# Kernel tuning notes

Measured on AMD Instinct MI355X. Metric: run time of the kernel, lower is better.

Reference implementation:

```python
import jax, jax.numpy as jnp
import numpy as np

C64 = jnp.complex64


def _rx(theta):
    # RX(t) = [[cos(t/2), -i sin(t/2)], [-i sin(t/2), cos(t/2)]]; theta scalar or [B]
    h = 0.5 * theta
    c = jnp.cos(h).astype(C64)
    s = (-1j * jnp.sin(h)).astype(C64)
    return jnp.stack([jnp.stack([c, s], -1), jnp.stack([s, c], -1)], -2)


def _ry(theta):
    h = 0.5 * theta
    c = jnp.cos(h).astype(C64)
    s = jnp.sin(h).astype(C64)
    return jnp.stack([jnp.stack([c, -s], -1), jnp.stack([s, c], -1)], -2)


def _rz(theta):
    h = 0.5 * theta
    em = jnp.exp(-1j * h).astype(C64)
    ep = jnp.exp(1j * h).astype(C64)
    z = jnp.zeros_like(em)
    return jnp.stack([jnp.stack([em, z], -1), jnp.stack([z, ep], -1)], -2)


def _apply_1q(state, U, q):
    # state: [B, 2^Q] complex; wire 0 is the most significant bit.
    B = state.shape[0]
    s = state.reshape(B, 2 ** q, 2, -1)
    if U.ndim == 3:  # batched gate [B,2,2]
        s = jnp.einsum('bij,bajc->baic', U, s)
    else:  # shared gate [2,2]
        s = jnp.einsum('ij,bajc->baic', U, s)
    return s.reshape(B, -1)


def _cnot_adj(state, q):
    # CNOT with control q, target q+1 (adjacent wires)
    B = state.shape[0]
    s = state.reshape(B, 2 ** q, 2, 2, -1)
    s = s.at[:, :, 1].set(s[:, :, 1, ::-1])
    return s.reshape(B, -1)


def _pqc(context, W, b, pqc_params):
    Q = W.shape[0]
    L = pqc_params.shape[0]
    angles = jnp.pi * jnp.tanh(context @ W.T + b)  # [B, Q]
    B = angles.shape[0]
    state = jnp.zeros((B, 2 ** Q), C64).at[:, 0].set(1.0)
    # data-encoding RX layer (batch-dependent angles)
    for q in range(Q):
        state = _apply_1q(state, _rx(angles[:, q]), q)
    # variational layers
    for l in range(L):
        for q in range(Q):
            state = _apply_1q(state, _rx(pqc_params[l, q, 0]), q)
            state = _apply_1q(state, _ry(pqc_params[l, q, 1]), q)
            state = _apply_1q(state, _rz(pqc_params[l, q, 2]), q)
        for q in range(Q - 1):
            state = _cnot_adj(state, q)
    # <Z_q> expectation for every wire
    probs = state.real ** 2 + state.imag ** 2  # [B, 2^Q]
    p = probs.reshape((B,) + (2,) * Q)
    z = [p.sum(tuple(i + 1 for i in range(Q) if i != q)) for q in range(Q)]  # each [B,2]
    z = jnp.stack(z, -1)  # [B, 2, Q] -> wait: stack of [B,2] on -1 -> [B,2,Q]
    return z[:, 0, :] - z[:, 1, :]  # [B, Q]


def setup_inputs() -> dict:
    key = jax.random.key(0)
    k0, k1, k2, k3 = jax.random.split(key, 4)
    B, D, Q, L = 512, 256, 16, 4
    context = jax.random.normal(k0, (B, D), jnp.float32)
    W = jax.random.normal(k1, (Q, D), jnp.float32) / np.float32(np.sqrt(D))
    b = 0.01 * jax.random.normal(k2, (Q,), jnp.float32)
    pqc_params = 0.01 * jax.random.normal(k3, (L, Q, 3), jnp.float32)
    return {"context": context, "W": W, "b": b, "pqc_params": pqc_params}


def reference(context, W, b, pqc_params):
    return _pqc(context, W, b, pqc_params)
```

## Files before the change

### kernel.cpp

```cpp
#include <hip/hip_runtime.h>
#include <math.h>

#define NQ   16
#define NTH  256
#define NB   512

typedef float2 c32;

__device__ __forceinline__ c32 cmul(c32 a, c32 b) {
    return make_float2(a.x*b.x - a.y*b.y, a.x*b.y + a.y*b.x);
}
__device__ __forceinline__ c32 cfma_(c32 a, c32 b, c32 acc) {
    acc.x = fmaf(a.x, b.x, fmaf(-a.y, b.y, acc.x));
    acc.y = fmaf(a.x, b.y, fmaf( a.y, b.x, acc.y));
    return acc;
}
__device__ __forceinline__ c32 cfmaConjA(c32 a, c32 b, c32 acc) {
    acc.x = fmaf(a.x, b.x, fmaf( a.y, b.y, acc.x));
    acc.y = fmaf(a.x, b.y, fmaf(-a.y, b.x, acc.y));
    return acc;
}
__device__ __forceinline__ c32 cmulConjA(c32 a, c32 b) {
    return cfmaConjA(a, b, make_float2(0.f, 0.f));
}
__device__ __forceinline__ c32 cadd(c32 a, c32 b){ return make_float2(a.x+b.x, a.y+b.y); }


__global__ __launch_bounds__(NTH, 2)
void pqc_mps_kernel(const float* __restrict__ ctx,
                    const float* __restrict__ Wm,
                    const float* __restrict__ bias,
                    const float* __restrict__ params,
                    float* __restrict__ out)
{
    __shared__ c32 Ac[14][272];
    __shared__ c32 A0c[16];
    __shared__ c32 A15v[32];
    __shared__ c32 Renv[15][144];
    __shared__ c32 Ssto[15][144];
    __shared__ c32 TR[272];
    __shared__ c32 TL[272];
    __shared__ c32 Lbuf[144];
    __shared__ c32 Ug[256];
    __shared__ c32 wv[64];
    __shared__ float angles[NQ];

    const int b = blockIdx.x;
    const int t = threadIdx.x;

    {
        const int q = t >> 4, g = t & 15;
        const float* crow = ctx + b * 256;
        const float* wrow = Wm + q * 256;
        float s = 0.f;
        #pragma unroll
        for (int j = 0; j < 16; ++j)
            s += crow[g + 16*j] * wrow[g + 16*j];
        #pragma unroll
        for (int m = 8; m; m >>= 1) s += __shfl_xor(s, m);
        if (g == 0) angles[q] = 3.14159265358979323846f * tanhf(s + bias[q]);
    }
    if (t < 64) {
        const float a  = params[t*3 + 0];
        const float bb = params[t*3 + 1];
        const float c  = params[t*3 + 2];
        const float ha = 0.5f*a, hb = 0.5f*bb, hc = 0.5f*c;
        const float ca = cosf(ha), sa = sinf(ha);
        const float cb = cosf(hb), sb = sinf(hb);
        const float cz = cosf(hc), sz = sinf(hc);
        const c32 m00 = make_float2( cb*ca,  sb*sa);
        const c32 m01 = make_float2(-sb*ca, -cb*sa);
        const c32 m10 = make_float2( sb*ca, -cb*sa);
        const c32 m11 = make_float2( cb*ca, -sb*sa);
        const c32 e0 = make_float2(cz, -sz);
        const c32 e1 = make_float2(cz,  sz);
        Ug[t*4 + 0] = cmul(e0, m00);
        Ug[t*4 + 1] = cmul(e0, m01);
        Ug[t*4 + 2] = cmul(e1, m10);
        Ug[t*4 + 3] = cmul(e1, m11);
    }
    __syncthreads();

    if (t < 64) {
        const int q = t >> 2, k = (t>>1)&1, i = t&1;
        const float h = 0.5f * angles[q];
        const float ch = cosf(h), sh = sinf(h);
        const int r0 = (i ^ k) << 1;
        const c32 u0 = Ug[(q<<2) + r0];
        const c32 u1 = Ug[(q<<2) + r0 + 1];
        wv[t] = make_float2(u0.x*ch + u1.y*sh, u0.y*ch - u1.x*sh);
    }
    __syncthreads();

    {
        const int r = t & 7, i = (t>>3)&1, a = t>>4;
        const int m0 = r&1, m1 = (r>>1)&1, m2 = r>>2;
        const int k0 = a&1, k1 = (a>>1)&1, k2 = (a>>2)&1, k3 = a>>3;
        #pragma unroll
        for (int q = 1; q <= 14; ++q) {
            const c32 u3 = Ug[((48+q)<<2) + ((i ^k3)<<1) + m2];
            const c32 u2 = Ug[((32+q)<<2) + ((m2^k2)<<1) + m1];
            const c32 u1 = Ug[((16+q)<<2) + ((m1^k1)<<1) + m0];
            const c32 ww = wv[(q<<2) + (k0<<1) + m0];
            Ac[q-1][a*17 + i*8 + r] = cmul(cmul(u3, u2), cmul(u1, ww));
        }
        if (t < 16) {
            const c32 u3 = Ug[(48<<2) + (i <<1) + m2];
            const c32 u2 = Ug[(32<<2) + (m2<<1) + m1];
            const c32 u1 = Ug[(16<<2) + (m1<<1) + m0];
            A0c[t] = cmul(cmul(u3, u2), cmul(u1, wv[m0]));
        }
        if (t >= 64 && t < 96) {
            const int idx = t - 64, aa = idx >> 1, ii = idx & 1;
            const int K0 = aa&1, K1 = (aa>>1)&1, K2 = (aa>>2)&1, K3 = aa>>3;
            c32 y1[2], y2[2];
            #pragma unroll
            for (int j1 = 0; j1 < 2; ++j1) {
                const int rr = (j1 ^ K1) << 1;
                y1[j1] = cfma_(Ug[((16+15)<<2)+rr], wv[60 + (K0<<1)],
                         cmul (Ug[((16+15)<<2)+rr+1], wv[60 + (K0<<1) + 1]));
            }
            #pragma unroll
            for (int j2 = 0; j2 < 2; ++j2) {
                const int rr = (j2 ^ K2) << 1;
                y2[j2] = cfma_(Ug[((32+15)<<2)+rr], y1[0],
                         cmul (Ug[((32+15)<<2)+rr+1], y1[1]));
            }
            const int rr = (ii ^ K3) << 1;
            A15v[(aa<<1)+ii] = cfma_(Ug[((48+15)<<2)+rr], y2[0],
                               cmul (Ug[((48+15)<<2)+rr+1], y2[1]));
        }
    }
    __syncthreads();

    if (t < 128) {
        const int m = t>>6, bl = (t>>3)&7, bp = t&7;
        c32 acc = cmulConjA(A15v[((m<<3)+bl)<<1],       A15v[((m<<3)+bp)<<1]);
        acc     = cfmaConjA(A15v[(((m<<3)+bl)<<1) + 1], A15v[(((m<<3)+bp)<<1) + 1], acc);
        Renv[14][m*72 + bl*9 + bp] = acc;
    } else {
        const int u = t-128, i = u>>6, bl = (u>>3)&7, bp = u&7;
        const c32 s = cmulConjA(A0c[(i<<3)+bl], A0c[(i<<3)+bp]);
        Ssto[0][i*72 + bl*9 + bp] = s;
        Lbuf   [i*72 + bl*9 + bp] = s;
    }
    __syncthreads();

    for (int s = 1; s <= 14; ++s) {
        const c32* Ap = Ac[14 - s];
        const c32* Rn = Renv[15 - s];
        const c32* As = Ac[s - 1];

        {
            const int bb = t>>4, i = (t>>3)&1, gp = t&7;
            const int m = bb>>3, al = bb&7;
            c32 tr = make_float2(0.f,0.f), tl = make_float2(0.f,0.f);
            #pragma unroll
            for (int g = 0; g < 8; ++g) {
                tr = cfmaConjA(Ap[bb*17 + i*8 + g], Rn[i*72 + g*9 + gp], tr);
                tl = cfma_(Lbuf[m*72 + al*9 + g], As[(m*8+g)*17 + i*8 + gp], tl);
            }
            TR[bb*17 + i*8 + gp] = tr;
            TL[bb*17 + i*8 + gp] = tl;
        }
        __syncthreads();

        if (t < 128) {
            const int m = t>>6, bl = (t>>3)&7, bp = t&7;
            const c32* trow = &TR[(m*8+bl)*17];
            const c32* arow = &Ap[(m*8+bp)*17];
            c32 r0 = make_float2(0.f,0.f), r1 = make_float2(0.f,0.f);
            #pragma unroll
            for (int ig = 0; ig < 16; ig += 2) {
                r0 = cfma_(trow[ig],   arow[ig],   r0);
                r1 = cfma_(trow[ig+1], arow[ig+1], r1);
            }
            Renv[14-s][m*72 + bl*9 + bp] = cadd(r0, r1);
        } else {
            const int u = t-128, i = u>>6, bl = (u>>3)&7, bp = u&7;
            c32 s0 = make_float2(0.f,0.f), s1 = make_float2(0.f,0.f);
            #pragma unroll
            for (int a = 0; a < 16; a += 2) {
                s0 = cfmaConjA(As[ a   *17 + i*8 + bl], TL[ a   *17 + i*8 + bp], s0);
                s1 = cfmaConjA(As[(a+1)*17 + i*8 + bl], TL[(a+1)*17 + i*8 + bp], s1);
            }
            const c32 sv = cadd(s0, s1);
            Ssto[s][i*72 + bl*9 + bp] = sv;
            Lbuf   [i*72 + bl*9 + bp] = sv;
        }
        __syncthreads();
    }

    {
        const int q = t >> 4, g = t & 15;
        float val = 0.f;
        if (q < 15) {
            const int i = g>>3, bl = g&7;
            const float sign = i ? -1.f : 1.f;
            const c32* Sq = &Ssto[q][i*72 + bl*9];
            const c32* Rq = &Renv[q][i*72 + bl*9];
            #pragma unroll
            for (int j = 0; j < 8; ++j)
                val += sign * (Sq[j].x*Rq[j].x - Sq[j].y*Rq[j].y);
        } else {
            const int m = g>>3, al = g&7;
            const c32 a0 = A15v[((m*8+al)<<1) + 0];
            const c32 a1 = A15v[((m*8+al)<<1) + 1];
            #pragma unroll
            for (int j = 0; j < 8; ++j) {
                c32 d = cmulConjA(a0, A15v[((m*8+j)<<1) + 0]);
                const c32 d1 = cmulConjA(a1, A15v[((m*8+j)<<1) + 1]);
                d.x -= d1.x; d.y -= d1.y;
                const c32 Lv = Lbuf[m*72 + al*9 + j];
                val += Lv.x*d.x - Lv.y*d.y;
            }
        }
        #pragma unroll
        for (int mm = 8; mm; mm >>= 1) val += __shfl_xor(val, mm);
        if (g == 0) out[b*NQ + q] = val;
    }
}

extern "C" void kernel_launch(void* const* d_in, const int* in_sizes, int n_in,
                              void* d_out, int out_size, void* d_ws, size_t ws_size,
                              hipStream_t stream) {
    const float* ctx    = (const float*)d_in[0];
    const float* Wm     = (const float*)d_in[1];
    const float* bias   = (const float*)d_in[2];
    const float* params = (const float*)d_in[3];
    float* out = (float*)d_out;
    (void)in_sizes; (void)n_in; (void)out_size; (void)d_ws; (void)ws_size;
    pqc_mps_kernel<<<NB, NTH, 0, stream>>>(ctx, Wm, bias, params, out);
}
```

Baseline: 79.42 us.

## Double block threads to split MPS contraction work across more lanes

Raises the block size from 256 to 512 threads and redistributes work. The angle dot product uses 32 lanes per qubit. Tensor construction is split in half across two thread groups, and the TR and TL contractions now run on separate halves. The env and S updates split each reduction across lane pairs and combine them with a shuffle. This shortens the serial per-step dependency chain in the 14-step sweep, at the cost of more threads per block, extra shuffles, and possibly lower register budget per thread.

```diff
diff --git a/kernel.cpp b/kernel.cpp
--- a/kernel.cpp
+++ b/kernel.cpp
@@ -2,7 +2,7 @@
 #include <math.h>
 
 #define NQ   16
-#define NTH  256
+#define NTH  512
 #define NB   512
 
 typedef float2 c32;
@@ -26,7 +26,7 @@
 __device__ __forceinline__ c32 cadd(c32 a, c32 b){ return make_float2(a.x+b.x, a.y+b.y); }
 
 
-__global__ __launch_bounds__(NTH, 2)
+__global__ __launch_bounds__(NTH, 4)
 void pqc_mps_kernel(const float* __restrict__ ctx,
                     const float* __restrict__ Wm,
                     const float* __restrict__ bias,
@@ -49,15 +49,15 @@
     const int t = threadIdx.x;
 
     {
-        const int q = t >> 4, g = t & 15;
+        const int q = t >> 5, g = t & 31;
         const float* crow = ctx + b * 256;
         const float* wrow = Wm + q * 256;
         float s = 0.f;
         #pragma unroll
-        for (int j = 0; j < 16; ++j)
-            s += crow[g + 16*j] * wrow[g + 16*j];
-        #pragma unroll
-        for (int m = 8; m; m >>= 1) s += __shfl_xor(s, m);
+        for (int j = 0; j < 8; ++j)
+            s += crow[g + 32*j] * wrow[g + 32*j];
+        #pragma unroll
+        for (int m = 16; m; m >>= 1) s += __shfl_xor(s, m);
         if (g == 0) angles[q] = 3.14159265358979323846f * tanhf(s + bias[q]);
     }
     if (t < 64) {
@@ -93,11 +93,12 @@
     __syncthreads();
 
     {
-        const int r = t & 7, i = (t>>3)&1, a = t>>4;
+        const int r = t & 7, i = (t>>3)&1, a = (t>>4)&15, h = t>>8;
         const int m0 = r&1, m1 = (r>>1)&1, m2 = r>>2;
         const int k0 = a&1, k1 = (a>>1)&1, k2 = (a>>2)&1, k3 = a>>3;
         #pragma unroll
-        for (int q = 1; q <= 14; ++q) {
+        for (int qq = 0; qq < 7; ++qq) {
+            const int q = 1 + h*7 + qq;
             const c32 u3 = Ug[((48+q)<<2) + ((i ^k3)<<1) + m2];
             const c32 u2 = Ug[((32+q)<<2) + ((m2^k2)<<1) + m1];
             const c32 u1 = Ug[((16+q)<<2) + ((m1^k1)<<1) + m0];
@@ -138,7 +139,7 @@
         c32 acc = cmulConjA(A15v[((m<<3)+bl)<<1],       A15v[((m<<3)+bp)<<1]);
         acc     = cfmaConjA(A15v[(((m<<3)+bl)<<1) + 1], A15v[(((m<<3)+bp)<<1) + 1], acc);
         Renv[14][m*72 + bl*9 + bp] = acc;
-    } else {
+    } else if (t < 256) {
         const int u = t-128, i = u>>6, bl = (u>>3)&7, bp = u&7;
         const c32 s = cmulConjA(A0c[(i<<3)+bl], A0c[(i<<3)+bp]);
         Ssto[0][i*72 + bl*9 + bp] = s;
@@ -151,47 +152,56 @@
         const c32* Rn = Renv[15 - s];
         const c32* As = Ac[s - 1];
 
-        {
+        if (t < 256) {
             const int bb = t>>4, i = (t>>3)&1, gp = t&7;
+            c32 tr = make_float2(0.f,0.f);
+            #pragma unroll
+            for (int g = 0; g < 8; ++g)
+                tr = cfmaConjA(Ap[bb*17 + i*8 + g], Rn[i*72 + g*9 + gp], tr);
+            TR[bb*17 + i*8 + gp] = tr;
+        } else {
+            const int u = t-256;
+            const int bb = u>>4, i = (u>>3)&1, gp = u&7;
             const int m = bb>>3, al = bb&7;
-            c32 tr = make_float2(0.f,0.f), tl = make_float2(0.f,0.f);
-            #pragma unroll
-            for (int g = 0; g < 8; ++g) {
-                tr = cfmaConjA(Ap[bb*17 + i*8 + g], Rn[i*72 + g*9 + gp], tr);
+            c32 tl = make_float2(0.f,0.f);
+            #pragma unroll
+            for (int g = 0; g < 8; ++g)
                 tl = cfma_(Lbuf[m*72 + al*9 + g], As[(m*8+g)*17 + i*8 + gp], tl);
-            }
-            TR[bb*17 + i*8 + gp] = tr;
             TL[bb*17 + i*8 + gp] = tl;
         }
         __syncthreads();
 
-        if (t < 128) {
-            const int m = t>>6, bl = (t>>3)&7, bp = t&7;
-            const c32* trow = &TR[(m*8+bl)*17];
-            const c32* arow = &Ap[(m*8+bp)*17];
-            c32 r0 = make_float2(0.f,0.f), r1 = make_float2(0.f,0.f);
-            #pragma unroll
-            for (int ig = 0; ig < 16; ig += 2) {
-                r0 = cfma_(trow[ig],   arow[ig],   r0);
-                r1 = cfma_(trow[ig+1], arow[ig+1], r1);
-            }
-            Renv[14-s][m*72 + bl*9 + bp] = cadd(r0, r1);
+        if (t < 256) {
+            const int i = t&1, bp = (t>>1)&7, bl = (t>>4)&7, m = (t>>7)&1;
+            const c32* trow = &TR[(m*8+bl)*17 + i*8];
+            const c32* arow = &Ap[(m*8+bp)*17 + i*8];
+            c32 r = make_float2(0.f,0.f);
+            #pragma unroll
+            for (int gp = 0; gp < 8; ++gp)
+                r = cfma_(trow[gp], arow[gp], r);
+            r.x += __shfl_xor(r.x, 1);
+            r.y += __shfl_xor(r.y, 1);
+            if (i == 0) Renv[14-s][m*72 + bl*9 + bp] = r;
         } else {
-            const int u = t-128, i = u>>6, bl = (u>>3)&7, bp = u&7;
-            c32 s0 = make_float2(0.f,0.f), s1 = make_float2(0.f,0.f);
-            #pragma unroll
-            for (int a = 0; a < 16; a += 2) {
-                s0 = cfmaConjA(As[ a   *17 + i*8 + bl], TL[ a   *17 + i*8 + bp], s0);
-                s1 = cfmaConjA(As[(a+1)*17 + i*8 + bl], TL[(a+1)*17 + i*8 + bp], s1);
-            }
-            const c32 sv = cadd(s0, s1);
-            Ssto[s][i*72 + bl*9 + bp] = sv;
-            Lbuf   [i*72 + bl*9 + bp] = sv;
+            const int u = t-256;
+            const int p = u&1, bp = (u>>1)&7, bl = (u>>4)&7, i = (u>>7)&1;
+            c32 sv = make_float2(0.f,0.f);
+            #pragma unroll
+            for (int a2 = 0; a2 < 8; ++a2) {
+                const int a = 2*a2 + p;
+                sv = cfmaConjA(As[a*17 + i*8 + bl], TL[a*17 + i*8 + bp], sv);
+            }
+            sv.x += __shfl_xor(sv.x, 1);
+            sv.y += __shfl_xor(sv.y, 1);
+            if (p == 0) {
+                Ssto[s][i*72 + bl*9 + bp] = sv;
+                Lbuf   [i*72 + bl*9 + bp] = sv;
+            }
         }
         __syncthreads();
     }
 
-    {
+    if (t < 256) {
         const int q = t >> 4, g = t & 15;
         float val = 0.f;
         if (q < 15) {
```

New measurement: 81.63 us. 2.8% more time.

## Run left/right environment sweeps in independent wavefronts without block barriers

Applied to the files above, without the earlier changes.

The 14-step left and right environment contractions previously used all 256 threads, with two block-wide barriers per step. Now each sweep runs on its own 32-lane group inside a single wavefront, and the two sweeps proceed in parallel with no intermediate __syncthreads. Each lane computes a register-blocked 2x2 or 4x2 tile, and intermediates are stored transposed or conjugated so the reads line up. This removes barrier latency and idle lanes, but puts eight times more serial arithmetic on each active lane. It also depends on implicit intra-wavefront ordering of shared-memory writes and reads.

```diff
diff --git a/kernel.cpp b/kernel.cpp
--- a/kernel.cpp
+++ b/kernel.cpp
@@ -23,7 +23,8 @@
 __device__ __forceinline__ c32 cmulConjA(c32 a, c32 b) {
     return cfmaConjA(a, b, make_float2(0.f, 0.f));
 }
-__device__ __forceinline__ c32 cadd(c32 a, c32 b){ return make_float2(a.x+b.x, a.y+b.y); }
+__device__ __forceinline__ c32 conjc(c32 a){ return make_float2(a.x, -a.y); }
+__device__ __forceinline__ c32 csub(c32 a, c32 b){ return make_float2(a.x-b.x, a.y-b.y); }
 
 
 __global__ __launch_bounds__(NTH, 2)
@@ -38,8 +39,8 @@
     __shared__ c32 A15v[32];
     __shared__ c32 Renv[15][144];
     __shared__ c32 Ssto[15][144];
-    __shared__ c32 TR[272];
-    __shared__ c32 TL[272];
+    __shared__ c32 TRb[272];
+    __shared__ c32 TLT[272];
     __shared__ c32 Lbuf[144];
     __shared__ c32 Ug[256];
     __shared__ c32 wv[64];
@@ -133,63 +134,126 @@
     }
     __syncthreads();
 
-    if (t < 128) {
-        const int m = t>>6, bl = (t>>3)&7, bp = t&7;
-        c32 acc = cmulConjA(A15v[((m<<3)+bl)<<1],       A15v[((m<<3)+bp)<<1]);
-        acc     = cfmaConjA(A15v[(((m<<3)+bl)<<1) + 1], A15v[(((m<<3)+bp)<<1) + 1], acc);
-        Renv[14][m*72 + bl*9 + bp] = acc;
-    } else {
-        const int u = t-128, i = u>>6, bl = (u>>3)&7, bp = u&7;
-        const c32 s = cmulConjA(A0c[(i<<3)+bl], A0c[(i<<3)+bp]);
-        Ssto[0][i*72 + bl*9 + bp] = s;
-        Lbuf   [i*72 + bl*9 + bp] = s;
-    }
-    __syncthreads();
-
-    for (int s = 1; s <= 14; ++s) {
-        const c32* Ap = Ac[14 - s];
-        const c32* Rn = Renv[15 - s];
-        const c32* As = Ac[s - 1];
-
-        {
-            const int bb = t>>4, i = (t>>3)&1, gp = t&7;
-            const int m = bb>>3, al = bb&7;
-            c32 tr = make_float2(0.f,0.f), tl = make_float2(0.f,0.f);
-            #pragma unroll
-            for (int g = 0; g < 8; ++g) {
-                tr = cfmaConjA(Ap[bb*17 + i*8 + g], Rn[i*72 + g*9 + gp], tr);
-                tl = cfma_(Lbuf[m*72 + al*9 + g], As[(m*8+g)*17 + i*8 + gp], tl);
-            }
-            TR[bb*17 + i*8 + gp] = tr;
-            TL[bb*17 + i*8 + gp] = tl;
-        }
-        __syncthreads();
-
-        if (t < 128) {
-            const int m = t>>6, bl = (t>>3)&7, bp = t&7;
-            const c32* trow = &TR[(m*8+bl)*17];
-            const c32* arow = &Ap[(m*8+bp)*17];
-            c32 r0 = make_float2(0.f,0.f), r1 = make_float2(0.f,0.f);
-            #pragma unroll
-            for (int ig = 0; ig < 16; ig += 2) {
-                r0 = cfma_(trow[ig],   arow[ig],   r0);
-                r1 = cfma_(trow[ig+1], arow[ig+1], r1);
-            }
-            Renv[14-s][m*72 + bl*9 + bp] = cadd(r0, r1);
-        } else {
-            const int u = t-128, i = u>>6, bl = (u>>3)&7, bp = u&7;
-            c32 s0 = make_float2(0.f,0.f), s1 = make_float2(0.f,0.f);
-            #pragma unroll
-            for (int a = 0; a < 16; a += 2) {
-                s0 = cfmaConjA(As[ a   *17 + i*8 + bl], TL[ a   *17 + i*8 + bp], s0);
-                s1 = cfmaConjA(As[(a+1)*17 + i*8 + bl], TL[(a+1)*17 + i*8 + bp], s1);
-            }
-            const c32 sv = cadd(s0, s1);
-            Ssto[s][i*72 + bl*9 + bp] = sv;
+    if (t < 64) {
+        #pragma unroll
+        for (int o = 0; o < 2; ++o) {
+            const int idx = t + 64*o;
+            const int m = idx>>6, bl = (idx>>3)&7, bp = idx&7;
+            c32 acc = cmulConjA(A15v[((m<<3)+bl)<<1],       A15v[((m<<3)+bp)<<1]);
+            acc     = cfmaConjA(A15v[(((m<<3)+bl)<<1) + 1], A15v[(((m<<3)+bp)<<1) + 1], acc);
+            Renv[14][m*72 + bl*9 + bp] = acc;
+        }
+        if (t < 32) {
+            const int bbq = t>>3, i1 = (t>>2)&1, gpp = t&3;
+            const int m2  = t>>4, blp = (t>>2)&3, bpp = t&3;
+            const int bl0 = 2*blp, bp0 = 2*bpp;
+            for (int s = 1; s <= 14; ++s) {
+                const c32* Ap = Ac[14 - s];
+                {
+                    const c32* RnB = Renv[15-s] + i1*72 + (2*gpp)*9;
+                    c32 rn0[8], rn1[8];
+                    #pragma unroll
+                    for (int g = 0; g < 8; ++g) { rn0[g] = RnB[g]; rn1[g] = RnB[9+g]; }
+                    #pragma unroll
+                    for (int b4 = 0; b4 < 4; ++b4) {
+                        const int bb = bbq*4 + b4;
+                        const c32* apr = Ap + bb*17 + i1*8;
+                        c32 a0 = make_float2(0.f,0.f), a1 = make_float2(0.f,0.f);
+                        #pragma unroll
+                        for (int g = 0; g < 8; ++g) {
+                            const c32 av = apr[g];
+                            a0 = cfma_(av, rn0[g], a0);
+                            a1 = cfma_(av, rn1[g], a1);
+                        }
+                        TRb[bb*17 + i1*8 + 2*gpp]     = conjc(a0);
+                        TRb[bb*17 + i1*8 + 2*gpp + 1] = conjc(a1);
+                    }
+                }
+                {
+                    const c32* tr0 = TRb + (m2*8 + bl0)*17;
+                    const c32* tr1 = tr0 + 17;
+                    const c32* ap0 = Ap + (m2*8 + bp0)*17;
+                    const c32* ap1 = ap0 + 17;
+                    c32 r00=make_float2(0.f,0.f), r01=r00, r10=r00, r11=r00;
+                    #pragma unroll
+                    for (int k = 0; k < 16; ++k) {
+                        const c32 t0 = tr0[k], t1 = tr1[k];
+                        const c32 p0 = ap0[k], p1 = ap1[k];
+                        r00 = cfma_(t0, p0, r00); r01 = cfma_(t0, p1, r01);
+                        r10 = cfma_(t1, p0, r10); r11 = cfma_(t1, p1, r11);
+                    }
+                    c32* Ro = Renv[14-s] + m2*72;
+                    Ro[ bl0   *9 + bp0] = r00; Ro[ bl0   *9 + bp0+1] = r01;
+                    Ro[(bl0+1)*9 + bp0] = r10; Ro[(bl0+1)*9 + bp0+1] = r11;
+                }
+            }
+        }
+    } else if (t < 128) {
+        const int u = t - 64;
+        #pragma unroll
+        for (int o = 0; o < 2; ++o) {
+            const int idx = u + 64*o;
+            const int i = idx>>6, bl = (idx>>3)&7, bp = idx&7;
+            const c32 sv = cmulConjA(A0c[(i<<3)+bl], A0c[(i<<3)+bp]);
+            Ssto[0][i*72 + bl*9 + bp] = sv;
             Lbuf   [i*72 + bl*9 + bp] = sv;
         }
-        __syncthreads();
-    }
+        if (u < 32) {
+            const int aq = u>>3, i1 = (u>>2)&1, bppA = u&3;
+            const int mL = aq>>1, al0 = (aq&1)*4, bp0 = 2*bppA;
+            const int i2 = u>>4, blp = (u>>2)&3, bppB = u&3;
+            const int bl0 = 2*blp, bq0 = 2*bppB;
+            for (int s = 1; s <= 14; ++s) {
+                const c32* As = Ac[s - 1];
+                {
+                    c32 lr[4][8];
+                    #pragma unroll
+                    for (int a4 = 0; a4 < 4; ++a4)
+                        #pragma unroll
+                        for (int g = 0; g < 8; ++g)
+                            lr[a4][g] = Lbuf[mL*72 + (al0+a4)*9 + g];
+                    c32 acc[4][2];
+                    #pragma unroll
+                    for (int a4 = 0; a4 < 4; ++a4) { acc[a4][0] = make_float2(0.f,0.f); acc[a4][1] = make_float2(0.f,0.f); }
+                    #pragma unroll
+                    for (int g = 0; g < 8; ++g) {
+                        const c32 s0 = As[(mL*8+g)*17 + i1*8 + bp0];
+                        const c32 s1 = As[(mL*8+g)*17 + i1*8 + bp0 + 1];
+                        #pragma unroll
+                        for (int a4 = 0; a4 < 4; ++a4) {
+                            acc[a4][0] = cfma_(lr[a4][g], s0, acc[a4][0]);
+                            acc[a4][1] = cfma_(lr[a4][g], s1, acc[a4][1]);
+                        }
+                    }
+                    #pragma unroll
+                    for (int a4 = 0; a4 < 4; ++a4) {
+                        TLT[(i1*8 + bp0    )*17 + aq*4 + a4] = acc[a4][0];
+                        TLT[(i1*8 + bp0 + 1)*17 + aq*4 + a4] = acc[a4][1];
+                    }
+                }
+                {
+                    const c32* tl0 = TLT + (i2*8 + bq0)*17;
+                    const c32* tl1 = tl0 + 17;
+                    c32 s00=make_float2(0.f,0.f), s01=s00, s10=s00, s11=s00;
+                    #pragma unroll
+                    for (int a = 0; a < 16; ++a) {
+                        const c32 x0 = As[a*17 + i2*8 + bl0];
+                        const c32 x1 = As[a*17 + i2*8 + bl0 + 1];
+                        const c32 t0 = tl0[a], t1 = tl1[a];
+                        s00 = cfmaConjA(x0, t0, s00); s01 = cfmaConjA(x0, t1, s01);
+                        s10 = cfmaConjA(x1, t0, s10); s11 = cfmaConjA(x1, t1, s11);
+                    }
+                    c32* So = Ssto[s] + i2*72;
+                    c32* Lo = Lbuf    + i2*72;
+                    So[ bl0   *9 + bq0] = s00; So[ bl0   *9 + bq0+1] = s01;
+                    So[(bl0+1)*9 + bq0] = s10; So[(bl0+1)*9 + bq0+1] = s11;
+                    Lo[ bl0   *9 + bq0] = s00; Lo[ bl0   *9 + bq0+1] = s01;
+                    Lo[(bl0+1)*9 + bq0] = s10; Lo[(bl0+1)*9 + bq0+1] = s11;
+                }
+            }
+        }
+    }
+    __syncthreads();
 
     {
         const int q = t >> 4, g = t & 15;
```

Result: slower. 84.80 us (+6.8%).

## Split MPS sweep stage by thread half with register prefetch of tensors

Applied to the files above, without the earlier changes.

The first stage of each sweep step is now split between thread halves. The lower 128 threads build the right transfer tensor and the upper 128 build the left one, each computing two outputs per thread, where before every thread computed both. Site-tensor operands for the next step and for the second stage are preloaded into registers before the barriers, so shared-memory load latency overlaps other work. The left intermediate is stored transposed to make the second-stage reads contiguous. This adds register pressure, which may lower occupancy under the 2-blocks launch bound.

```diff
diff --git a/kernel.cpp b/kernel.cpp
--- a/kernel.cpp
+++ b/kernel.cpp
@@ -23,6 +23,7 @@
 __device__ __forceinline__ c32 cmulConjA(c32 a, c32 b) {
     return cfmaConjA(a, b, make_float2(0.f, 0.f));
 }
+__device__ __forceinline__ c32 conjc(c32 a){ return make_float2(a.x, -a.y); }
 __device__ __forceinline__ c32 cadd(c32 a, c32 b){ return make_float2(a.x+b.x, a.y+b.y); }
 
 
@@ -38,8 +39,8 @@
     __shared__ c32 A15v[32];
     __shared__ c32 Renv[15][144];
     __shared__ c32 Ssto[15][144];
-    __shared__ c32 TR[272];
-    __shared__ c32 TL[272];
+    __shared__ c32 TRb[272];
+    __shared__ c32 TLT[272];
     __shared__ c32 Lbuf[144];
     __shared__ c32 Ug[256];
     __shared__ c32 wv[64];
@@ -133,60 +134,102 @@
     }
     __syncthreads();
 
+    const int bbR = t >> 3, iR = (t >> 2) & 1, gp0 = (t & 3) * 2;
+    const int uL = t - 128;
+    const int aL = uL >> 3, iL = (uL >> 2) & 1, bp0 = (uL & 3) * 2;
+    const int mL = aL >> 3, alL = aL & 7;
+    const int m2 = (t >> 6) & 1, bl2 = (t >> 3) & 7, bp2 = t & 7;
+    const int i2L = uL >> 6;
+
+    c32 aP1[8], sA0[8], sA1[8], pf2[16];
+
     if (t < 128) {
         const int m = t>>6, bl = (t>>3)&7, bp = t&7;
         c32 acc = cmulConjA(A15v[((m<<3)+bl)<<1],       A15v[((m<<3)+bp)<<1]);
         acc     = cfmaConjA(A15v[(((m<<3)+bl)<<1) + 1], A15v[(((m<<3)+bp)<<1) + 1], acc);
         Renv[14][m*72 + bl*9 + bp] = acc;
+        const c32* Ap = Ac[13];
+        #pragma unroll
+        for (int g = 0; g < 8; ++g) aP1[g] = Ap[bbR*17 + iR*8 + g];
     } else {
-        const int u = t-128, i = u>>6, bl = (u>>3)&7, bp = u&7;
-        const c32 s = cmulConjA(A0c[(i<<3)+bl], A0c[(i<<3)+bp]);
-        Ssto[0][i*72 + bl*9 + bp] = s;
-        Lbuf   [i*72 + bl*9 + bp] = s;
+        const int i = uL>>6, bl = (uL>>3)&7, bp = uL&7;
+        const c32 sv = cmulConjA(A0c[(i<<3)+bl], A0c[(i<<3)+bp]);
+        Ssto[0][i*72 + bl*9 + bp] = sv;
+        Lbuf   [i*72 + bl*9 + bp] = sv;
+        const c32* As = Ac[0];
+        #pragma unroll
+        for (int g = 0; g < 8; ++g) {
+            sA0[g] = As[(mL*8+g)*17 + iL*8 + bp0];
+            sA1[g] = As[(mL*8+g)*17 + iL*8 + bp0 + 1];
+        }
     }
     __syncthreads();
 
     for (int s = 1; s <= 14; ++s) {
         const c32* Ap = Ac[14 - s];
-        const c32* Rn = Renv[15 - s];
         const c32* As = Ac[s - 1];
 
-        {
-            const int bb = t>>4, i = (t>>3)&1, gp = t&7;
-            const int m = bb>>3, al = bb&7;
-            c32 tr = make_float2(0.f,0.f), tl = make_float2(0.f,0.f);
+        if (t < 128) {
+            const c32* RnB = Renv[15-s] + iR*72 + gp0*9;
+            c32 x0 = make_float2(0.f,0.f), x1 = x0;
             #pragma unroll
             for (int g = 0; g < 8; ++g) {
-                tr = cfmaConjA(Ap[bb*17 + i*8 + g], Rn[i*72 + g*9 + gp], tr);
-                tl = cfma_(Lbuf[m*72 + al*9 + g], As[(m*8+g)*17 + i*8 + gp], tl);
-            }
-            TR[bb*17 + i*8 + gp] = tr;
-            TL[bb*17 + i*8 + gp] = tl;
+                x0 = cfma_(aP1[g], RnB[g],   x0);
+                x1 = cfma_(aP1[g], RnB[9+g], x1);
+            }
+            TRb[bbR*17 + iR*8 + gp0]     = conjc(x0);
+            TRb[bbR*17 + iR*8 + gp0 + 1] = conjc(x1);
+            #pragma unroll
+            for (int k = 0; k < 16; ++k) pf2[k] = Ap[(m2*8+bp2)*17 + k];
+        } else {
+            const c32* Lr = Lbuf + mL*72 + alL*9;
+            c32 x0 = make_float2(0.f,0.f), x1 = x0;
+            #pragma unroll
+            for (int g = 0; g < 8; ++g) {
+                const c32 lv = Lr[g];
+                x0 = cfma_(lv, sA0[g], x0);
+                x1 = cfma_(lv, sA1[g], x1);
+            }
+            TLT[(iL*8 + bp0    )*17 + aL] = x0;
+            TLT[(iL*8 + bp0 + 1)*17 + aL] = x1;
+            #pragma unroll
+            for (int k = 0; k < 16; ++k) pf2[k] = As[k*17 + i2L*8 + bl2];
         }
         __syncthreads();
 
         if (t < 128) {
-            const int m = t>>6, bl = (t>>3)&7, bp = t&7;
-            const c32* trow = &TR[(m*8+bl)*17];
-            const c32* arow = &Ap[(m*8+bp)*17];
-            c32 r0 = make_float2(0.f,0.f), r1 = make_float2(0.f,0.f);
-            #pragma unroll
-            for (int ig = 0; ig < 16; ig += 2) {
-                r0 = cfma_(trow[ig],   arow[ig],   r0);
-                r1 = cfma_(trow[ig+1], arow[ig+1], r1);
-            }
-            Renv[14-s][m*72 + bl*9 + bp] = cadd(r0, r1);
+            const c32* trR = TRb + (m2*8 + bl2)*17;
+            c32 r0 = make_float2(0.f,0.f), r1 = r0;
+            #pragma unroll
+            for (int k = 0; k < 16; k += 2) {
+                r0 = cfma_(trR[k],   pf2[k],   r0);
+                r1 = cfma_(trR[k+1], pf2[k+1], r1);
+            }
+            Renv[14-s][m2*72 + bl2*9 + bp2] = cadd(r0, r1);
+            if (s < 14) {
+                const c32* ApN = Ac[13 - s];
+                #pragma unroll
+                for (int g = 0; g < 8; ++g) aP1[g] = ApN[bbR*17 + iR*8 + g];
+            }
         } else {
-            const int u = t-128, i = u>>6, bl = (u>>3)&7, bp = u&7;
-            c32 s0 = make_float2(0.f,0.f), s1 = make_float2(0.f,0.f);
-            #pragma unroll
-            for (int a = 0; a < 16; a += 2) {
-                s0 = cfmaConjA(As[ a   *17 + i*8 + bl], TL[ a   *17 + i*8 + bp], s0);
-                s1 = cfmaConjA(As[(a+1)*17 + i*8 + bl], TL[(a+1)*17 + i*8 + bp], s1);
+            const c32* tlR = TLT + (i2L*8 + bp2)*17;
+            c32 s0 = make_float2(0.f,0.f), s1 = s0;
+            #pragma unroll
+            for (int k = 0; k < 16; k += 2) {
+                s0 = cfmaConjA(pf2[k],   tlR[k],   s0);
+                s1 = cfmaConjA(pf2[k+1], tlR[k+1], s1);
             }
             const c32 sv = cadd(s0, s1);
-            Ssto[s][i*72 + bl*9 + bp] = sv;
-            Lbuf   [i*72 + bl*9 + bp] = sv;
+            Ssto[s][i2L*72 + bl2*9 + bp2] = sv;
+            Lbuf   [i2L*72 + bl2*9 + bp2] = sv;
+            if (s < 14) {
+                const c32* AsN = Ac[s];
+                #pragma unroll
+                for (int g = 0; g < 8; ++g) {
+                    sA0[g] = AsN[(mL*8+g)*17 + iL*8 + bp0];
+                    sA1[g] = AsN[(mL*8+g)*17 + iL*8 + bp0 + 1];
+                }
+            }
         }
         __syncthreads();
     }
```

Measured after the change: 78.06 us. Within noise of the previous version (-1.7%).
